# Optimization experiments

Hardware: AMD Instinct MI355X
Metric: run time of the kernel (lower is better)

## Reference

```python
import jax, jax.numpy as jnp
import numpy as np

H, D, K = 8, 512, 64
EPS = 1e-12


def _l2norm(x):
    # F.normalize(p=2, dim=-1): x / max(||x||_2, eps)
    n = jnp.sqrt(jnp.sum(x * x, axis=-1, keepdims=True))
    return x / jnp.maximum(n, EPS)


def setup_inputs() -> dict:
    key = jax.random.key(0)
    ks = jax.random.split(key, 8)
    S, B = 1024, 16
    scale = 1.0 / np.sqrt(D)
    return {
        "query": jax.random.normal(ks[0], (S, B, D), dtype=jnp.float32),
        "key": jax.random.normal(ks[1], (S, B, D), dtype=jnp.float32),
        "value": jax.random.normal(ks[2], (S, B, D), dtype=jnp.float32),
        # stacked per-head projection weights, torch Linear convention [out,in]
        "WQ": jax.random.uniform(ks[3], (H, K, D), jnp.float32, -scale, scale),
        "WK": jax.random.uniform(ks[4], (H, K, D), jnp.float32, -scale, scale),
        "WV": jax.random.uniform(ks[5], (H, K, D), jnp.float32, -scale, scale),
        "Wout": jax.random.uniform(ks[6], (D, H * K), jnp.float32,
                                   -1.0 / np.sqrt(H * K), 1.0 / np.sqrt(H * K)),
    }


def reference(query, key, value, WQ, WK, WV, Wout):
    temp = K ** 0.5
    # project all heads at once: [S,B,D] x [H,K,D] -> [B,H,S,K]
    wq = _l2norm(jnp.einsum("sbd,hkd->bhsk", query, WQ))
    wk = _l2norm(jnp.einsum("sbd,hkd->bhsk", key, WK))
    wv = _l2norm(jnp.einsum("sbd,hkd->bhsk", value, WV))
    # cosine-similarity attention scores [B,H,Sq,Sk]
    scores = jnp.einsum("bhsk,bhtk->bhst", wq, wk) / temp
    aff = jax.nn.softmax(scores, axis=-1)
    out = jnp.einsum("bhst,bhtk->bhsk", aff, wv)  # [B,H,S,K]
    # concat heads -> [S,B,H*K] (matches torch per-head concat on last dim)
    Sq, B = query.shape[0], query.shape[1]
    concat = out.transpose(2, 0, 1, 3).reshape(Sq, B, H * K)
    return concat @ Wout.T  # [S,B,D]
```

## Files before the change

### kernel.cpp

```cpp
#include <hip/hip_runtime.h>
#include <cstdint>
#include <cstddef>

typedef unsigned int u32;
typedef unsigned short u16;
typedef __attribute__((ext_vector_type(8))) short short8;
typedef __attribute__((ext_vector_type(4))) float f32x4;

#define S_LEN 1024
#define BATCH 16
#define NHEAD 8
#define DMODEL 512
#define KHD 64
#define NROW (S_LEN * BATCH)

__device__ __forceinline__ u16 f2bf(float f) {
    u32 u = __float_as_uint(f);
    return (u16)((u + 0x7fffu + ((u >> 16) & 1u)) >> 16);
}

__device__ __forceinline__ void gl_lds16(const void* g, void* l) {
    __builtin_amdgcn_global_load_lds(
        (const __attribute__((address_space(1))) void*)(uintptr_t)g,
        (__attribute__((address_space(3))) void*)(uintptr_t)l, 16, 0, 0);
}

__global__ __launch_bounds__(256) void wcvt_kernel(
    const float* __restrict__ WQ, const float* __restrict__ WK,
    const float* __restrict__ WV, const float* __restrict__ Wo,
    u16* __restrict__ dst)
{
    const int m = blockIdx.y;
    const float* __restrict__ src = (m == 0) ? WQ : (m == 1) ? WK : (m == 2) ? WV : Wo;
    const int idx = (blockIdx.x * 256 + threadIdx.x) * 4;
    const float4 v = *(const float4*)(src + idx);
    u16 r[4];
    r[0] = f2bf(v.x); r[1] = f2bf(v.y); r[2] = f2bf(v.z); r[3] = f2bf(v.w);
    *(uint2*)(dst + (size_t)m * DMODEL * DMODEL + idx) = *(uint2*)r;
}

__global__ __launch_bounds__(256) void xcvt_kernel(
    const float* __restrict__ s0, const float* __restrict__ s1,
    u16* __restrict__ dst)
{
    const float* __restrict__ src = (blockIdx.y == 0) ? s0 : s1;
    u16* d = dst + (size_t)blockIdx.y * NROW * DMODEL;
    const int idx = (blockIdx.x * 256 + threadIdx.x) * 4;
    const float4 v = *(const float4*)(src + idx);
    u16 r[4];
    r[0] = f2bf(v.x); r[1] = f2bf(v.y); r[2] = f2bf(v.z); r[3] = f2bf(v.w);
    *(uint2*)(d + idx) = *(uint2*)r;
}

template<int M>
__global__ __launch_bounds__(256) void gemm_kernel(
    const u16* __restrict__ Abf,
    const u16* __restrict__ Wb,
    u16* __restrict__ outN,
    float* __restrict__ outP)
{
    __shared__ __align__(16) u16 Alds[128 * 64];
    __shared__ __align__(16) u16 Blds[128 * 64];

    const int tid  = threadIdx.x;
    const int wave = tid >> 6;
    const int lane = tid & 63;
    const int m16  = lane & 15;
    const int quad = lane >> 4;
    const int wm   = wave >> 1;
    const int wn   = wave & 1;
    const int n0   = blockIdx.y * 128;
    const int row0 = blockIdx.x * 128;
    const int z    = (M == 1) ? blockIdx.z : 0;
    const int bb   = (M == 2) ? blockIdx.z : 0;

    const u16* __restrict__ A = Abf + (size_t)z * NROW * DMODEL + (size_t)bb * DMODEL;
    const size_t astr = (M == 2) ? (size_t)BATCH * DMODEL : (size_t)DMODEL;
    const u16* __restrict__ B = Wb + ((M == 1) ? (size_t)z * DMODEL * DMODEL : 0);

    f32x4 acc[4][4] = {};

    const int brow   = lane >> 3;
    const int bchunk = (lane & 7) ^ brow;

    for (int kt = 0; kt < DMODEL; kt += 64) {
        __syncthreads();
        {
            u16* la = &Alds[(wave * 32) * 64];
            u16* lb = &Blds[(wave * 32) * 64];
            const u16* bp = B + (size_t)(n0 + wave * 32 + brow) * DMODEL + kt + bchunk * 8;
            if (M == 0) {
                const int colc = kt + bchunk * 8;
                const int hh   = colc >> 6;
                const int kk   = colc & 63;
#pragma unroll
                for (int j = 0; j < 4; j++) {
                    const int i  = row0 + wave * 32 + brow + j * 8;
                    const int ss = i >> 4, bx = i & 15;
                    gl_lds16(Abf + (((size_t)(bx * NHEAD + hh) * S_LEN + ss) * KHD + kk),
                             la + j * 8 * 64);
                    gl_lds16(bp + (size_t)j * 8 * DMODEL, lb + j * 8 * 64);
                }
            } else {
                const u16* ap = A + (size_t)(row0 + wave * 32 + brow) * astr + kt + bchunk * 8;
#pragma unroll
                for (int j = 0; j < 4; j++) {
                    gl_lds16(ap + (size_t)j * 8 * astr,   la + j * 8 * 64);
                    gl_lds16(bp + (size_t)j * 8 * DMODEL, lb + j * 8 * 64);
                }
            }
        }
        __syncthreads();

#pragma unroll
        for (int half = 0; half < 2; half++) {
            short8 af[4], bfr[4];
#pragma unroll
            for (int mt = 0; mt < 4; mt++)
                af[mt] = *(const short8*)&Alds[(wm * 64 + mt * 16 + m16) * 64 +
                                               (((half << 2) + quad) ^ (m16 & 7)) * 8];
#pragma unroll
            for (int nt = 0; nt < 4; nt++)
                bfr[nt] = *(const short8*)&Blds[(wn * 64 + nt * 16 + m16) * 64 +
                                                (((half << 2) + quad) ^ (m16 & 7)) * 8];
#pragma unroll
            for (int mt = 0; mt < 4; mt++)
#pragma unroll
                for (int nt = 0; nt < 4; nt++)
                    acc[mt][nt] = __builtin_amdgcn_mfma_f32_16x16x32_bf16(af[mt], bfr[nt], acc[mt][nt], 0, 0, 0);
        }
    }

    if (M == 1) {
        const int h = (n0 >> 6) + wn;
        u16* outZ = outN + (size_t)z * BATCH * NHEAD * S_LEN * KHD;
#pragma unroll
        for (int mt = 0; mt < 4; mt++) {
#pragma unroll
            for (int r = 0; r < 4; r++) {
                float ss = 0.0f;
#pragma unroll
                for (int nt = 0; nt < 4; nt++) ss += acc[mt][nt][r] * acc[mt][nt][r];
                ss += __shfl_xor(ss, 1);
                ss += __shfl_xor(ss, 2);
                ss += __shfl_xor(ss, 4);
                ss += __shfl_xor(ss, 8);
                const float sc = 1.0f / fmaxf(sqrtf(ss), 1e-12f);
                const int i = row0 + wm * 64 + mt * 16 + quad * 4 + r;
                const int s = i >> 4, b = i & 15;
                u16* op = outZ + (((size_t)b * NHEAD + h) * S_LEN + s) * KHD;
#pragma unroll
                for (int nt = 0; nt < 4; nt++)
                    op[nt * 16 + m16] = f2bf(acc[mt][nt][r] * sc);
            }
        }
    } else if (M == 2) {
        const int h = (n0 >> 6) + wn;
#pragma unroll
        for (int mt = 0; mt < 4; mt++) {
            float scl[4];
#pragma unroll
            for (int r = 0; r < 4; r++) {
                float ss = 0.0f;
#pragma unroll
                for (int nt = 0; nt < 4; nt++) ss += acc[mt][nt][r] * acc[mt][nt][r];
                ss += __shfl_xor(ss, 1);
                ss += __shfl_xor(ss, 2);
                ss += __shfl_xor(ss, 4);
                ss += __shfl_xor(ss, 8);
                scl[r] = 1.0f / fmaxf(sqrtf(ss), 1e-12f);
            }
            const int sbase = row0 + wm * 64 + mt * 16 + quad * 4;
#pragma unroll
            for (int nt = 0; nt < 4; nt++) {
                const int vcol = nt * 16 + m16;
                uint2 pk;
                pk.x = (u32)f2bf(acc[mt][nt][0] * scl[0]) |
                       ((u32)f2bf(acc[mt][nt][1] * scl[1]) << 16);
                pk.y = (u32)f2bf(acc[mt][nt][2] * scl[2]) |
                       ((u32)f2bf(acc[mt][nt][3] * scl[3]) << 16);
                u16* dp = outN + (((size_t)bb * NHEAD + h) * KHD + vcol) * S_LEN + sbase;
                *(uint2*)dp = pk;
            }
        }
    } else {
#pragma unroll
        for (int mt = 0; mt < 4; mt++) {
#pragma unroll
            for (int r = 0; r < 4; r++) {
                const int i = row0 + wm * 64 + mt * 16 + quad * 4 + r;
                float* op = outP + (size_t)i * DMODEL + n0 + wn * 64;
#pragma unroll
                for (int nt = 0; nt < 4; nt++)
                    op[nt * 16 + m16] = acc[mt][nt][r];
            }
        }
    }
}

__global__ __launch_bounds__(256, 2) void attn_kernel(
    const u16* __restrict__ wq, const u16* __restrict__ wk, const u16* __restrict__ wvT,
    u16* __restrict__ Xout)
{
    __shared__ __align__(16) u16 Klds[2][64 * 64];
    __shared__ __align__(16) u16 Vlds[2][64 * 64];
    __shared__ __align__(16) u16 Plds[4][4][16 * 32];

    const int tid  = threadIdx.x;
    const int wave = tid >> 6;
    const int lane = tid & 63;
    const int m16  = lane & 15;
    const int quad = lane >> 4;
    const int bh   = blockIdx.x;
    const int qt   = blockIdx.y;

    const u16* Qb = wq  + (size_t)bh * S_LEN * KHD;
    const u16* Kb = wk  + (size_t)bh * S_LEN * KHD;
    const u16* Vb = wvT + (size_t)bh * KHD * S_LEN;

    const int qr0 = qt * 256 + wave * 64;
    short8 qf[4][2];
#pragma unroll
    for (int qb = 0; qb < 4; qb++) {
        qf[qb][0] = *(const short8*)(Qb + (size_t)(qr0 + qb * 16 + m16) * KHD + quad * 8);
        qf[qb][1] = *(const short8*)(Qb + (size_t)(qr0 + qb * 16 + m16) * KHD + 32 + quad * 8);
    }

    short8 ones;
#pragma unroll
    for (int j = 0; j < 8; j++) ones[j] = (short)0x3F80;

    f32x4 o[4][4] = {};
    f32x4 ls[4]   = {};
    const float C1 = 0.125f, C2 = 0.0078125f;

    const int srow   = lane >> 3;
    const int schunk = (lane & 7) ^ srow;
    const int r0     = wave * 8 + srow;
    const int pswz   = (m16 >> 1) & 3;

    gl_lds16(Kb + (size_t)r0 * KHD + schunk * 8,               &Klds[0][(wave * 8) * 64]);
    gl_lds16(Kb + (size_t)(r0 + 32) * KHD + schunk * 8,        &Klds[0][(wave * 8 + 32) * 64]);
    gl_lds16(Vb + (size_t)r0 * S_LEN + schunk * 8,             &Vlds[0][(wave * 8) * 64]);
    gl_lds16(Vb + (size_t)(r0 + 32) * S_LEN + schunk * 8,      &Vlds[0][(wave * 8 + 32) * 64]);
    __syncthreads();

    for (int it = 0; it < S_LEN / 64; it++) {
        const int cur = it & 1;

        if (it + 1 < S_LEN / 64) {
            const int nxt = cur ^ 1;
            const int kt0 = (it + 1) * 64;
            gl_lds16(Kb + (size_t)(kt0 + r0) * KHD + schunk * 8,        &Klds[nxt][(wave * 8) * 64]);
            gl_lds16(Kb + (size_t)(kt0 + r0 + 32) * KHD + schunk * 8,   &Klds[nxt][(wave * 8 + 32) * 64]);
            gl_lds16(Vb + (size_t)r0 * S_LEN + kt0 + schunk * 8,        &Vlds[nxt][(wave * 8) * 64]);
            gl_lds16(Vb + (size_t)(r0 + 32) * S_LEN + kt0 + schunk * 8, &Vlds[nxt][(wave * 8 + 32) * 64]);
        }

#pragma unroll
        for (int cc = 0; cc < 2; cc++) {
#pragma unroll
            for (int mm = 0; mm < 2; mm++) {
                const int mt = cc * 2 + mm;
                const short8 kf0 = *(const short8*)&Klds[cur][(mt * 16 + m16) * 64 + (quad ^ (m16 & 7)) * 8];
                const short8 kf1 = *(const short8*)&Klds[cur][(mt * 16 + m16) * 64 + ((4 + quad) ^ (m16 & 7)) * 8];
#pragma unroll
                for (int qb = 0; qb < 4; qb++) {
                    f32x4 s = {};
                    s = __builtin_amdgcn_mfma_f32_16x16x32_bf16(kf0, qf[qb][0], s, 0, 0, 0);
                    s = __builtin_amdgcn_mfma_f32_16x16x32_bf16(kf1, qf[qb][1], s, 0, 0, 0);
                    u32 up[4];
#pragma unroll
                    for (int r = 0; r < 4; r++) {
                        const float y = s[r];
                        const float p = fmaf(fmaf(C2, y, C1), y, 1.0f);
                        up[r] = __float_as_uint(p);
                    }
                    uint2 pk;
                    pk.x = __builtin_amdgcn_perm(up[1], up[0], 0x07060302u);
                    pk.y = __builtin_amdgcn_perm(up[3], up[2], 0x07060302u);
                    *(uint2*)((char*)&Plds[wave][qb][0] + m16 * 64 +
                              ((((mm << 1) + (quad >> 1)) ^ pswz) << 4) + ((quad & 1) << 3)) = pk;
                }
            }

            short8 vfr[4];
#pragma unroll
            for (int vt = 0; vt < 4; vt++)
                vfr[vt] = *(const short8*)&Vlds[cur][(vt * 16 + m16) * 64 +
                                                     (((cc << 2) + quad) ^ (m16 & 7)) * 8];
            __builtin_amdgcn_s_setprio(1);
#pragma unroll
            for (int qb = 0; qb < 4; qb++) {
                const short8 pb = *(const short8*)((const char*)&Plds[wave][qb][0] + m16 * 64 +
                                                   ((quad ^ pswz) << 4));
                ls[qb] = __builtin_amdgcn_mfma_f32_16x16x32_bf16(ones, pb, ls[qb], 0, 0, 0);
#pragma unroll
                for (int vt = 0; vt < 4; vt++)
                    o[qb][vt] = __builtin_amdgcn_mfma_f32_16x16x32_bf16(vfr[vt], pb, o[qb][vt], 0, 0, 0);
            }
            __builtin_amdgcn_s_setprio(0);
        }

        __syncthreads();
    }

    u16* outB = Xout + (size_t)bh * S_LEN * KHD;
#pragma unroll
    for (int qb = 0; qb < 4; qb++) {
        const float inv = 1.0f / ls[qb][0];
        const int qrow = qr0 + qb * 16 + m16;
        u16* cp = outB + (size_t)qrow * KHD;
#pragma unroll
        for (int vt = 0; vt < 4; vt++) {
            uint2 pk;
            pk.x = (u32)f2bf(o[qb][vt][0] * inv) | ((u32)f2bf(o[qb][vt][1] * inv) << 16);
            pk.y = (u32)f2bf(o[qb][vt][2] * inv) | ((u32)f2bf(o[qb][vt][3] * inv) << 16);
            *(uint2*)(cp + vt * 16 + quad * 4) = pk;
        }
    }
}

extern "C" void kernel_launch(void* const* d_in, const int* in_sizes, int n_in,
                              void* d_out, int out_size, void* d_ws, size_t ws_size,
                              hipStream_t stream) {
    const float* q    = (const float*)d_in[0];
    const float* k    = (const float*)d_in[1];
    const float* v    = (const float*)d_in[2];
    const float* WQ   = (const float*)d_in[3];
    const float* WK   = (const float*)d_in[4];
    const float* WV   = (const float*)d_in[5];
    const float* Wout = (const float*)d_in[6];
    float* out = (float*)d_out;
    u16*  Xbf = (u16*)d_out;

    const size_t per = (size_t)BATCH * NHEAD * S_LEN * KHD;
    u16* wsQKV = (u16*)d_ws;
    u16* wsW   = wsQKV + 3 * per;

    wcvt_kernel<<<dim3(256, 4), 256, 0, stream>>>(WQ, WK, WV, Wout, wsW);

    xcvt_kernel<<<dim3(NROW * DMODEL / 1024, 2), 256, 0, stream>>>(q, k, Xbf);

    gemm_kernel<1><<<dim3(NROW / 128, DMODEL / 128, 2), 256, 0, stream>>>(
        Xbf, wsW, wsQKV, nullptr);

    xcvt_kernel<<<dim3(NROW * DMODEL / 1024, 1), 256, 0, stream>>>(v, v, Xbf);

    gemm_kernel<2><<<dim3(S_LEN / 128, DMODEL / 128, BATCH), 256, 0, stream>>>(
        Xbf, wsW + (size_t)2 * DMODEL * DMODEL, wsQKV + 2 * per, nullptr);

    attn_kernel<<<dim3(BATCH * NHEAD, S_LEN / 256), 256, 0, stream>>>(
        wsQKV, wsQKV + per, wsQKV + 2 * per, wsQKV);

    gemm_kernel<0><<<dim3(NROW / 128, DMODEL / 128, 1), 256, 0, stream>>>(
        wsQKV, wsW + (size_t)3 * DMODEL * DMODEL, nullptr, out);
}
```

Baseline: 250.8 us.

## Retile attention: 128-query blocks, 128-key tiles, software-pipelined PV stage

The attention kernel now gives each block 128 query rows (32 per wave) instead of 256, which doubles the grid, and stages 128-key K/V tiles per iteration with a new V swizzle. The P tile is double-buffered so the P·V MFMAs for one 32-key chunk run while the next chunk's scores are computed. This aims to raise occupancy and overlap the score and PV phases, at the cost of more K/V reloads per query and more LDS per block.

```diff
diff --git a/kernel.cpp b/kernel.cpp
--- a/kernel.cpp
+++ b/kernel.cpp
@@ -202,9 +202,9 @@
     const u16* __restrict__ wq, const u16* __restrict__ wk, const u16* __restrict__ wvT,
     u16* __restrict__ Xout)
 {
-    __shared__ __align__(16) u16 Klds[2][64 * 64];
-    __shared__ __align__(16) u16 Vlds[2][64 * 64];
-    __shared__ __align__(16) u16 Plds[4][4][16 * 32];
+    __shared__ __align__(16) u16 Klds[2][128 * 64];
+    __shared__ __align__(16) u16 Vlds[2][64 * 128];
+    __shared__ __align__(16) u16 Plds[4][2][2][16 * 32];
 
     const int tid  = threadIdx.x;
     const int wave = tid >> 6;
@@ -218,10 +218,10 @@
     const u16* Kb = wk  + (size_t)bh * S_LEN * KHD;
     const u16* Vb = wvT + (size_t)bh * KHD * S_LEN;
 
-    const int qr0 = qt * 256 + wave * 64;
-    short8 qf[4][2];
-#pragma unroll
-    for (int qb = 0; qb < 4; qb++) {
+    const int qr0 = qt * 128 + wave * 32;
+    short8 qf[2][2];
+#pragma unroll
+    for (int qb = 0; qb < 2; qb++) {
         qf[qb][0] = *(const short8*)(Qb + (size_t)(qr0 + qb * 16 + m16) * KHD + quad * 8);
         qf[qb][1] = *(const short8*)(Qb + (size_t)(qr0 + qb * 16 + m16) * KHD + 32 + quad * 8);
     }
@@ -230,42 +230,53 @@
 #pragma unroll
     for (int j = 0; j < 8; j++) ones[j] = (short)0x3F80;
 
-    f32x4 o[4][4] = {};
-    f32x4 ls[4]   = {};
+    f32x4 o[2][4] = {};
+    f32x4 ls[2]   = {};
     const float C1 = 0.125f, C2 = 0.0078125f;
 
     const int srow   = lane >> 3;
     const int schunk = (lane & 7) ^ srow;
-    const int r0     = wave * 8 + srow;
+    const int kr0    = wave * 8 + srow;
+    const int vsub   = lane >> 4;
+    const int vslot  = lane & 15;
     const int pswz   = (m16 >> 1) & 3;
 
-    gl_lds16(Kb + (size_t)r0 * KHD + schunk * 8,               &Klds[0][(wave * 8) * 64]);
-    gl_lds16(Kb + (size_t)(r0 + 32) * KHD + schunk * 8,        &Klds[0][(wave * 8 + 32) * 64]);
-    gl_lds16(Vb + (size_t)r0 * S_LEN + schunk * 8,             &Vlds[0][(wave * 8) * 64]);
-    gl_lds16(Vb + (size_t)(r0 + 32) * S_LEN + schunk * 8,      &Vlds[0][(wave * 8 + 32) * 64]);
+#define STAGE_TILE(kt0, b)                                                          \
+    {                                                                               \
+        _Pragma("unroll")                                                           \
+        for (int j = 0; j < 4; j++)                                                 \
+            gl_lds16(Kb + (size_t)((kt0) + kr0 + j * 32) * KHD + schunk * 8,        \
+                     &Klds[b][(wave * 8 + j * 32) * 64]);                           \
+        _Pragma("unroll")                                                           \
+        for (int j = 0; j < 4; j++) {                                               \
+            const int vb = wave * 16 + j * 4;                                       \
+            const int v  = vb + vsub;                                               \
+            gl_lds16(Vb + (size_t)v * S_LEN + (kt0) + (vslot ^ (v & 15)) * 8,       \
+                     &Vlds[b][vb * 128]);                                           \
+        }                                                                           \
+    }
+
+    STAGE_TILE(0, 0)
     __syncthreads();
 
-    for (int it = 0; it < S_LEN / 64; it++) {
+    for (int it = 0; it < S_LEN / 128; it++) {
         const int cur = it & 1;
 
-        if (it + 1 < S_LEN / 64) {
-            const int nxt = cur ^ 1;
-            const int kt0 = (it + 1) * 64;
-            gl_lds16(Kb + (size_t)(kt0 + r0) * KHD + schunk * 8,        &Klds[nxt][(wave * 8) * 64]);
-            gl_lds16(Kb + (size_t)(kt0 + r0 + 32) * KHD + schunk * 8,   &Klds[nxt][(wave * 8 + 32) * 64]);
-            gl_lds16(Vb + (size_t)r0 * S_LEN + kt0 + schunk * 8,        &Vlds[nxt][(wave * 8) * 64]);
-            gl_lds16(Vb + (size_t)(r0 + 32) * S_LEN + kt0 + schunk * 8, &Vlds[nxt][(wave * 8 + 32) * 64]);
-        }
-
-#pragma unroll
-        for (int cc = 0; cc < 2; cc++) {
+        if (it + 1 < S_LEN / 128) {
+            STAGE_TILE((it + 1) * 128, cur ^ 1)
+        }
+
+#pragma unroll
+        for (int cc = 0; cc < 4; cc++) {
 #pragma unroll
             for (int mm = 0; mm < 2; mm++) {
                 const int mt = cc * 2 + mm;
-                const short8 kf0 = *(const short8*)&Klds[cur][(mt * 16 + m16) * 64 + (quad ^ (m16 & 7)) * 8];
-                const short8 kf1 = *(const short8*)&Klds[cur][(mt * 16 + m16) * 64 + ((4 + quad) ^ (m16 & 7)) * 8];
-#pragma unroll
-                for (int qb = 0; qb < 4; qb++) {
+                const short8 kf0 = *(const short8*)&Klds[cur][(mt * 16 + m16) * 64 +
+                                                              (quad ^ (m16 & 7)) * 8];
+                const short8 kf1 = *(const short8*)&Klds[cur][(mt * 16 + m16) * 64 +
+                                                              ((4 + quad) ^ (m16 & 7)) * 8];
+#pragma unroll
+                for (int qb = 0; qb < 2; qb++) {
                     f32x4 s = {};
                     s = __builtin_amdgcn_mfma_f32_16x16x32_bf16(kf0, qf[qb][0], s, 0, 0, 0);
                     s = __builtin_amdgcn_mfma_f32_16x16x32_bf16(kf1, qf[qb][1], s, 0, 0, 0);
@@ -279,21 +290,44 @@
                     uint2 pk;
                     pk.x = __builtin_amdgcn_perm(up[1], up[0], 0x07060302u);
                     pk.y = __builtin_amdgcn_perm(up[3], up[2], 0x07060302u);
-                    *(uint2*)((char*)&Plds[wave][qb][0] + m16 * 64 +
+                    *(uint2*)((char*)&Plds[wave][cc & 1][qb][0] + m16 * 64 +
                               ((((mm << 1) + (quad >> 1)) ^ pswz) << 4) + ((quad & 1) << 3)) = pk;
                 }
             }
 
+            if (cc > 0) {
+                const int c = cc - 1;
+                short8 vfr[4];
+#pragma unroll
+                for (int vt = 0; vt < 4; vt++)
+                    vfr[vt] = *(const short8*)&Vlds[cur][(vt * 16 + m16) * 128 +
+                                                         (((c << 2) + quad) ^ m16) * 8];
+                __builtin_amdgcn_s_setprio(1);
+#pragma unroll
+                for (int qb = 0; qb < 2; qb++) {
+                    const short8 pb = *(const short8*)((const char*)&Plds[wave][c & 1][qb][0] +
+                                                       m16 * 64 + ((quad ^ pswz) << 4));
+                    ls[qb] = __builtin_amdgcn_mfma_f32_16x16x32_bf16(ones, pb, ls[qb], 0, 0, 0);
+#pragma unroll
+                    for (int vt = 0; vt < 4; vt++)
+                        o[qb][vt] = __builtin_amdgcn_mfma_f32_16x16x32_bf16(vfr[vt], pb, o[qb][vt], 0, 0, 0);
+                }
+                __builtin_amdgcn_s_setprio(0);
+            }
+        }
+
+        {
+            const int c = 3;
             short8 vfr[4];
 #pragma unroll
             for (int vt = 0; vt < 4; vt++)
-                vfr[vt] = *(const short8*)&Vlds[cur][(vt * 16 + m16) * 64 +
-                                                     (((cc << 2) + quad) ^ (m16 & 7)) * 8];
+                vfr[vt] = *(const short8*)&Vlds[cur][(vt * 16 + m16) * 128 +
+                                                     (((c << 2) + quad) ^ m16) * 8];
             __builtin_amdgcn_s_setprio(1);
 #pragma unroll
-            for (int qb = 0; qb < 4; qb++) {
-                const short8 pb = *(const short8*)((const char*)&Plds[wave][qb][0] + m16 * 64 +
-                                                   ((quad ^ pswz) << 4));
+            for (int qb = 0; qb < 2; qb++) {
+                const short8 pb = *(const short8*)((const char*)&Plds[wave][c & 1][qb][0] +
+                                                   m16 * 64 + ((quad ^ pswz) << 4));
                 ls[qb] = __builtin_amdgcn_mfma_f32_16x16x32_bf16(ones, pb, ls[qb], 0, 0, 0);
 #pragma unroll
                 for (int vt = 0; vt < 4; vt++)
@@ -304,10 +338,11 @@
 
         __syncthreads();
     }
+#undef STAGE_TILE
 
     u16* outB = Xout + (size_t)bh * S_LEN * KHD;
 #pragma unroll
-    for (int qb = 0; qb < 4; qb++) {
+    for (int qb = 0; qb < 2; qb++) {
         const float inv = 1.0f / ls[qb][0];
         const int qrow = qr0 + qb * 16 + m16;
         u16* cp = outB + (size_t)qrow * KHD;
@@ -350,7 +385,7 @@
     gemm_kernel<2><<<dim3(S_LEN / 128, DMODEL / 128, BATCH), 256, 0, stream>>>(
         Xbf, wsW + (size_t)2 * DMODEL * DMODEL, wsQKV + 2 * per, nullptr);
 
-    attn_kernel<<<dim3(BATCH * NHEAD, S_LEN / 256), 256, 0, stream>>>(
+    attn_kernel<<<dim3(BATCH * NHEAD, S_LEN / 128), 256, 0, stream>>>(
         wsQKV, wsQKV + per, wsQKV + 2 * per, wsQKV);
 
     gemm_kernel<0><<<dim3(NROW / 128, DMODEL / 128, 1), 256, 0, stream>>>(
```

Result: slower. 256.3 us (+2.2%).
